# Performance work log

Measured on AMD Instinct MI355X. Metric: run time of the kernel, lower is better.

Reference implementation:

```python
import jax, jax.numpy as jnp
import numpy as np
jax.config.update("jax_enable_x64", True)

B, N, S, H, D = 64, 13, 128, 768, 512
MAX_DEPTH = 8
MAX_SHAPE_IDS = 256  # min(2**13, 256)


def _gelu(x):
    return jax.nn.gelu(x, approximate=False)  # torch nn.GELU default (erf)


def setup_inputs() -> dict:
    key = jax.random.key(0)
    ks = jax.random.split(key, 12)
    # BFS-complete binary tree with 13 nodes: nodes 0..5 internal, 6..12 leaves
    left = np.array([2 * i + 1 if 2 * i + 2 < N else -1 for i in range(N)], dtype=np.int64)
    right = np.array([2 * i + 2 if 2 * i + 2 < N else -1 for i in range(N)], dtype=np.int64)
    depth = np.array([int(np.floor(np.log2(i + 1))) for i in range(N)], dtype=np.int64)
    is_leaf = np.tile((left == -1)[None, :], (B, 1))  # (B, N) bool
    active = np.ones((B, N), dtype=bool)
    leaf_states = jax.random.normal(ks[0], (B, N, S, H), dtype=jnp.float32)
    leaf_masks = jax.random.bernoulli(ks[1], 0.8, (B, N, S))  # bool
    s = 0.02
    params = dict(
        Wl1=jax.random.normal(ks[2], (H, D), dtype=jnp.float32) * s,
        bl1=jnp.zeros((D,), jnp.float32),
        Wl2=jax.random.normal(ks[3], (D, D), dtype=jnp.float32) * s,
        bl2=jnp.zeros((D,), jnp.float32),
        Wm1=jax.random.normal(ks[4], (2 * D, D), dtype=jnp.float32) * s,
        bm1=jnp.zeros((D,), jnp.float32),
        Wm2=jax.random.normal(ks[5], (D, D), dtype=jnp.float32) * s,
        bm2=jnp.zeros((D,), jnp.float32),
        depth_emb=jax.random.normal(ks[6], (MAX_DEPTH, D), dtype=jnp.float32) * s,
        shape_emb=jax.random.normal(ks[7], (MAX_SHAPE_IDS, D), dtype=jnp.float32) * s,
    )
    return dict(is_leaf=is_leaf, active=active, depth=depth, left_child=left,
                right_child=right, leaf_states=leaf_states, leaf_masks=leaf_masks,
                **params)


def reference(is_leaf, active, depth, left_child, right_child, leaf_states, leaf_masks,
              Wl1, bl1, Wl2, bl2, Wm1, bm1, Wm2, bm2, depth_emb, shape_emb):
    is_leaf = jnp.asarray(is_leaf)
    active = jnp.asarray(active)
    # --- leaf pass (vectorized over all nodes) ---
    maskf = leaf_masks[..., None].astype(leaf_states.dtype)          # (B,N,S,1)
    pooled = (leaf_states * maskf).sum(2) / jnp.maximum(maskf.sum(2), 1.0)  # (B,N,H)
    enc = _gelu(pooled @ Wl1 + bl1) @ Wl2 + bl2                       # (B,N,D)
    enc = enc + depth_emb[jnp.asarray(depth)][None, :, :]             # per-node depth embed
    node_repr = enc * is_leaf[..., None].astype(enc.dtype)            # zero non-leaves
    # --- bottom-up merge (small fixed loop over max_nodes, reverse BFS) ---
    lc_np = np.asarray(left_child)
    rc_np = np.asarray(right_child)
    dp_np = np.asarray(depth)
    for i in range(N - 1, -1, -1):
        lc, rc = int(lc_np[i]), int(rc_np[i])
        if lc == -1:
            continue
        is_internal = active[:, i] & ~is_leaf[:, i]                   # (B,)
        cat = jnp.concatenate([node_repr[:, lc], node_repr[:, rc]], axis=-1)  # (B,2D)
        merged = _gelu(cat @ Wm1 + bm1) @ Wm2 + bm2 + depth_emb[int(dp_np[i])]
        # torch code overwrites the whole column with merged*mask iff any internal
        col = jnp.where(jnp.any(is_internal),
                        merged * is_internal[:, None].astype(merged.dtype),
                        node_repr[:, i])
        node_repr = node_repr.at[:, i].set(col)
    # --- topology hash -> shape embedding ---
    pattern = active.astype(jnp.int64) * 2 + is_leaf.astype(jnp.int64)  # (B,N)
    weights = jnp.array([31 ** i for i in range(N)], dtype=jnp.int64)    # fits int64 for N<=13
    hashed = jnp.abs((pattern * weights[None, :]).sum(1)) % MAX_SHAPE_IDS
    return node_repr[:, 0] + shape_emb[hashed]
```

## Files before the change

### kernel.cpp

```cpp
#include <hip/hip_runtime.h>
#include <hip/hip_bf16.h>
#include <math.h>

#define NN 13
#define SS 128
#define HH 768
#define DD 512

typedef __attribute__((ext_vector_type(8))) short bf16x8;
typedef __attribute__((ext_vector_type(4))) float f32x4;

__device__ __forceinline__ float gelu_f(float x) {
    return 0.5f * x * (1.0f + erff(x * 0.7071067811865475f));
}
__device__ __forceinline__ ushort f2b(float v) {
    __hip_bfloat16 h = __float2bfloat16(v);
    return *reinterpret_cast<ushort*>(&h);
}
__device__ __forceinline__ float b2f(ushort u) {
    __hip_bfloat16 h = *reinterpret_cast<__hip_bfloat16*>(&u);
    return __bfloat162float(h);
}

__device__ __forceinline__ int shape_hash(const int* __restrict__ active,
                                          const int* __restrict__ is_leaf, int b) {
    unsigned long long acc = 0ull, w = 1ull;
    for (int i = 0; i < NN; ++i) {
        unsigned long long p = (unsigned long long)(active[b*NN + i] * 2 + is_leaf[b*NN + i]);
        acc += p * w;
        w *= 31ull;
    }
    long long h = (long long)acc;
    if (h < 0) h = -h;
    return (int)(h % 256);
}

__global__ __launch_bounds__(192)
void pool_partial(const float* __restrict__ ls, const int* __restrict__ masks,
                  const int* __restrict__ is_leaf,
                  float* __restrict__ part, float* __restrict__ cntbuf)
{
    int idx = blockIdx.x;
    int R = idx >> 2, q = idx & 3;
    int n = R >> 6, b = R & 63;
    if (!is_leaf[b*NN + n]) return;
    const float4* src = (const float4*)(ls + (size_t)(b*NN + n) * SS * HH + (size_t)q * 32 * HH);
    const int* mk = masks + (b*NN + n) * SS + q * 32;
    int t = threadIdx.x;

    __shared__ float lsm[32];
    if (t < 32) lsm[t] = (float)mk[t];
    __syncthreads();

    float4 a = {0.f, 0.f, 0.f, 0.f};
    float cnt = 0.f;
    #pragma unroll 16
    for (int s = 0; s < 32; ++s) {
        float m = lsm[s];
        float4 v = src[s * (HH/4) + t];
        a.x += m * v.x; a.y += m * v.y; a.z += m * v.z; a.w += m * v.w;
        cnt += m;
    }
    ((float4*)(part + ((size_t)q * 832 + R) * HH))[t] = a;
    if (t == 0) cntbuf[q * 832 + R] = cnt;
}

__global__ __launch_bounds__(256)
void combine_transpose(const float* __restrict__ part, const float* __restrict__ cntbuf,
                       const int* __restrict__ is_leaf, ushort* __restrict__ pooled,
                       const float* __restrict__ Wl1, const float* __restrict__ Wl2,
                       const float* __restrict__ Wm1, const float* __restrict__ Wm2,
                       ushort* __restrict__ Tl1, ushort* __restrict__ Tl2,
                       ushort* __restrict__ Tm1, ushort* __restrict__ Tm2)
{
    int bx = blockIdx.x;
    if (bx < 832) {
        int u = bx;
        int n = u >> 6, b = u & 63;
        int t = threadIdx.x;
        if (t >= 192) return;
        ushort4* dst = (ushort4*)(pooled + (size_t)u * HH);
        if (!is_leaf[b*NN + n]) {
            ushort4 z = {0, 0, 0, 0};
            dst[t] = z;
            return;
        }
        float cnt = cntbuf[u] + cntbuf[832+u] + cntbuf[1664+u] + cntbuf[2496+u];
        float inv = 1.f / fmaxf(cnt, 1.f);
        float4 s = {0.f, 0.f, 0.f, 0.f};
        #pragma unroll
        for (int q = 0; q < 4; ++q) {
            float4 v = ((const float4*)(part + ((size_t)q * 832 + u) * HH))[t];
            s.x += v.x; s.y += v.y; s.z += v.z; s.w += v.w;
        }
        ushort4 o = { f2b(s.x*inv), f2b(s.y*inv), f2b(s.z*inv), f2b(s.w*inv) };
        dst[t] = o;
        return;
    }
    int tb = bx - 832;
    const float* W; ushort* T; int K, tile;
    if (tb < 384)       { W = Wl1; T = Tl1; K = 768;  tile = tb; }
    else if (tb < 640)  { W = Wl2; T = Tl2; K = 512;  tile = tb - 384; }
    else if (tb < 1152) { W = Wm1; T = Tm1; K = 1024; tile = tb - 640; }
    else                { W = Wm2; T = Tm2; K = 512;  tile = tb - 1152; }
    int tk = tile >> 4, tj = tile & 15;
    __shared__ float lds[32][33];
    int t = threadIdx.x;
    int r = t >> 3, c0 = (t & 7) * 4;
    const float4 v = *(const float4*)(W + (size_t)(tk*32 + r)*DD + tj*32 + c0);
    lds[r][c0+0] = v.x; lds[r][c0+1] = v.y; lds[r][c0+2] = v.z; lds[r][c0+3] = v.w;
    __syncthreads();
    ushort* dst = T + (size_t)(tj*32 + r)*K + tk*32 + c0;
    dst[0] = f2b(lds[c0+0][r]); dst[1] = f2b(lds[c0+1][r]);
    dst[2] = f2b(lds[c0+2][r]); dst[3] = f2b(lds[c0+3][r]);
}

enum { LEAF_G1 = 0, LEAF_G2 = 1, MERGE_G1 = 2, MERGE_G2 = 3, FINAL_G2 = 4 };

template<int MODE, int KT>
__global__ __launch_bounds__(256)
void mfma_gemm(const ushort* __restrict__ Asrc, const ushort* __restrict__ WT,
               const float* __restrict__ bias, void* __restrict__ CoutV,
               const int* __restrict__ is_leaf, const int* __restrict__ active,
               const int* __restrict__ depth, const int* __restrict__ left,
               const int* __restrict__ right,
               const float* __restrict__ depth_emb, const float* __restrict__ shape_emb,
               const ushort* __restrict__ noderep,
               int n0, int n1, int n2)
{
    constexpr int NITER = KT / 32;
    __shared__ ushort a_lds[2][64*40];
    __shared__ ushort b_lds[2][64*40];

    const int t = threadIdx.x;
    const int lane = t & 63, wv = t >> 6;
    const int j0 = blockIdx.x * 64;
    const int by = blockIdx.y;
    const int lrow = lane & 15, lhi = lane >> 4;

    int node, lc = 0, rc = 0;
    if (MODE == LEAF_G1 || MODE == LEAF_G2) {
        node = by;
        bool anyleaf = __any(is_leaf[lane*NN + node] != 0);
        if (!anyleaf) {
            if (MODE == LEAF_G2) {
                ushort* dst = (ushort*)CoutV + (size_t)(node*64)*DD;
                #pragma unroll
                for (int c = 0; c < 4; ++c) {
                    int jc = j0 + c*16 + lrow;
                    #pragma unroll
                    for (int reg = 0; reg < 4; ++reg) {
                        int rw = wv*16 + lhi*4 + reg;
                        dst[(size_t)rw*DD + jc] = 0;
                    }
                }
            }
            return;
        }
    } else {
        node = (by == 0) ? n0 : ((by == 1) ? n1 : n2);
        lc = left[node]; rc = right[node];
    }

    const int AK = (MODE == LEAF_G1) ? HH : DD;
    const int rowbase = (MODE == LEAF_G1 || MODE == LEAF_G2) ? node*64
                       : (MODE == MERGE_G1) ? 0 : by*64;

    const int sr = t >> 2, skg = t & 3;
    f32x4 acc[4];
    #pragma unroll
    for (int c = 0; c < 4; ++c) acc[c] = (f32x4){0.f, 0.f, 0.f, 0.f};

    auto addrA = [&](int kt) -> const ushort* {
        int k0 = kt*32 + skg*8;
        if (MODE == MERGE_G1) {
            return (k0 < DD) ? noderep + (size_t)(lc*64 + sr)*DD + k0
                             : noderep + (size_t)(rc*64 + sr)*DD + (k0 - DD);
        }
        return Asrc + (size_t)(rowbase + sr)*AK + k0;
    };
    auto addrB = [&](int kt) -> const ushort* {
        return WT + (size_t)(j0 + sr)*KT + kt*32 + skg*8;
    };

    uint4 aR0, bR0, aR1, bR1;
    auto load0 = [&](int kt) { aR0 = *(const uint4*)addrA(kt); bR0 = *(const uint4*)addrB(kt); };
    auto load1 = [&](int kt) { aR1 = *(const uint4*)addrA(kt); bR1 = *(const uint4*)addrB(kt); };
    auto store0 = [&](int buf) {
        *(uint4*)&a_lds[buf][sr*40 + skg*8] = aR0;
        *(uint4*)&b_lds[buf][sr*40 + skg*8] = bR0;
    };
    auto store1 = [&](int buf) {
        *(uint4*)&a_lds[buf][sr*40 + skg*8] = aR1;
        *(uint4*)&b_lds[buf][sr*40 + skg*8] = bR1;
    };
    auto computeOn = [&](const ushort* aL, const ushort* bL) {
        bf16x8 af = *(const bf16x8*)&aL[(wv*16 + lrow)*40 + lhi*8];
        #pragma unroll
        for (int c = 0; c < 4; ++c) {
            bf16x8 bfr = *(const bf16x8*)&bL[(c*16 + lrow)*40 + lhi*8];
            acc[c] = __builtin_amdgcn_mfma_f32_16x16x32_bf16(af, bfr, acc[c], 0, 0, 0);
        }
    };

    load0(0);
    store0(0);
    if (NITER > 1) load1(1);
    __syncthreads();

    for (int kt = 0; kt < NITER; kt += 2) {
        computeOn(a_lds[0], b_lds[0]);
        if (kt + 2 < NITER) load0(kt + 2);
        store1(1);
        __syncthreads();
        computeOn(a_lds[1], b_lds[1]);
        if (kt + 3 < NITER) load1(kt + 3);
        if (kt + 2 < NITER) store0(0);
        __syncthreads();
    }

    if (MODE == LEAF_G1) {
        ushort* H = (ushort*)CoutV + (size_t)(node*64)*DD;
        #pragma unroll
        for (int c = 0; c < 4; ++c) {
            int jc = j0 + c*16 + lrow;
            float bj = bias[jc];
            #pragma unroll
            for (int reg = 0; reg < 4; ++reg) {
                int rw = wv*16 + lhi*4 + reg;
                H[(size_t)rw*DD + jc] = f2b(gelu_f(acc[c][reg] + bj));
            }
        }
    } else if (MODE == LEAF_G2) {
        int dp = depth[node];
        const float* de = depth_emb + (size_t)dp*DD;
        bool lf[4];
        #pragma unroll
        for (int reg = 0; reg < 4; ++reg)
            lf[reg] = is_leaf[(wv*16 + lhi*4 + reg)*NN + node] != 0;
        ushort* dst = (ushort*)CoutV + (size_t)(node*64)*DD;
        #pragma unroll
        for (int c = 0; c < 4; ++c) {
            int jc = j0 + c*16 + lrow;
            float bj = bias[jc] + de[jc];
            #pragma unroll
            for (int reg = 0; reg < 4; ++reg) {
                int rw = wv*16 + lhi*4 + reg;
                dst[(size_t)rw*DD + jc] = f2b(lf[reg] ? (acc[c][reg] + bj) : 0.f);
            }
        }
    } else if (MODE == MERGE_G1) {
        ushort* Mh = (ushort*)CoutV + (size_t)(by*64)*DD;
        #pragma unroll
        for (int c = 0; c < 4; ++c) {
            int jc = j0 + c*16 + lrow;
            float bj = bias[jc];
            #pragma unroll
            for (int reg = 0; reg < 4; ++reg) {
                int rw = wv*16 + lhi*4 + reg;
                Mh[(size_t)rw*DD + jc] = f2b(gelu_f(acc[c][reg] + bj));
            }
        }
    } else {
        int dp = depth[node];
        const float* de = depth_emb + (size_t)dp*DD;
        bool anyInt = __any(active[lane*NN + node] && !is_leaf[lane*NN + node]);
        bool iv[4];
        #pragma unroll
        for (int reg = 0; reg < 4; ++reg) {
            int rw = wv*16 + lhi*4 + reg;
            iv[reg] = active[rw*NN + node] && !is_leaf[rw*NN + node];
        }
        if (MODE == MERGE_G2) {
            if (!anyInt) return;
            ushort* dst = (ushort*)CoutV + (size_t)(node*64)*DD;
            #pragma unroll
            for (int c = 0; c < 4; ++c) {
                int jc = j0 + c*16 + lrow;
                float bj = bias[jc] + de[jc];
                #pragma unroll
                for (int reg = 0; reg < 4; ++reg) {
                    int rw = wv*16 + lhi*4 + reg;
                    dst[(size_t)rw*DD + jc] = f2b(iv[reg] ? (acc[c][reg] + bj) : 0.f);
                }
            }
        } else {
            float* out = (float*)CoutV;
            int hh[4];
            #pragma unroll
            for (int reg = 0; reg < 4; ++reg)
                hh[reg] = shape_hash(active, is_leaf, wv*16 + lhi*4 + reg);
            #pragma unroll
            for (int c = 0; c < 4; ++c) {
                int jc = j0 + c*16 + lrow;
                float bj = bias[jc] + de[jc];
                #pragma unroll
                for (int reg = 0; reg < 4; ++reg) {
                    int rw = wv*16 + lhi*4 + reg;
                    float base = anyInt ? (iv[reg] ? (acc[c][reg] + bj) : 0.f)
                                        : b2f(noderep[(size_t)(node*64 + rw)*DD + jc]);
                    out[(size_t)rw*DD + jc] = base + shape_emb[(size_t)hh[reg]*DD + jc];
                }
            }
        }
    }
}

extern "C" void kernel_launch(void* const* d_in, const int* in_sizes, int n_in,
                              void* d_out, int out_size, void* d_ws, size_t ws_size,
                              hipStream_t stream)
{
    const int*   is_leaf     = (const int*)d_in[0];
    const int*   active      = (const int*)d_in[1];
    const int*   depth       = (const int*)d_in[2];
    const int*   left        = (const int*)d_in[3];
    const int*   right       = (const int*)d_in[4];
    const float* leaf_states = (const float*)d_in[5];
    const int*   leaf_masks  = (const int*)d_in[6];
    const float* Wl1 = (const float*)d_in[7];
    const float* bl1 = (const float*)d_in[8];
    const float* Wl2 = (const float*)d_in[9];
    const float* bl2 = (const float*)d_in[10];
    const float* Wm1 = (const float*)d_in[11];
    const float* bm1 = (const float*)d_in[12];
    const float* Wm2 = (const float*)d_in[13];
    const float* bm2 = (const float*)d_in[14];
    const float* depth_emb = (const float*)d_in[15];
    const float* shape_emb = (const float*)d_in[16];
    float* out = (float*)d_out;

    float* part   = (float*)d_ws;
    float* cntbuf = part + 4*832*768;
    ushort* pooled  = (ushort*)(cntbuf + 4*832);
    ushort* hidden  = pooled + 832*768;
    ushort* noderep = hidden + 832*512;
    ushort* mhid    = noderep + 832*512;
    ushort* Tl1 = mhid + 3*64*512;
    ushort* Tl2 = Tl1 + 512*768;
    ushort* Tm1 = Tl2 + 512*512;
    ushort* Tm2 = Tm1 + 512*1024;

    pool_partial<<<832*4, 192, 0, stream>>>(leaf_states, leaf_masks, is_leaf, part, cntbuf);
    combine_transpose<<<832 + 1408, 256, 0, stream>>>(part, cntbuf, is_leaf, pooled,
                                                      Wl1, Wl2, Wm1, Wm2, Tl1, Tl2, Tm1, Tm2);

    mfma_gemm<LEAF_G1, 768><<<dim3(8, 13), 256, 0, stream>>>(
        pooled, Tl1, bl1, hidden, is_leaf, active, depth, left, right,
        depth_emb, shape_emb, noderep, 0, 0, 0);
    mfma_gemm<LEAF_G2, 512><<<dim3(8, 13), 256, 0, stream>>>(
        hidden, Tl2, bl2, noderep, is_leaf, active, depth, left, right,
        depth_emb, shape_emb, noderep, 0, 0, 0);

    mfma_gemm<MERGE_G1, 1024><<<dim3(8, 3), 256, 0, stream>>>(
        nullptr, Tm1, bm1, mhid, is_leaf, active, depth, left, right,
        depth_emb, shape_emb, noderep, 3, 4, 5);
    mfma_gemm<MERGE_G2, 512><<<dim3(8, 3), 256, 0, stream>>>(
        mhid, Tm2, bm2, noderep, is_leaf, active, depth, left, right,
        depth_emb, shape_emb, noderep, 3, 4, 5);

    mfma_gemm<MERGE_G1, 1024><<<dim3(8, 2), 256, 0, stream>>>(
        nullptr, Tm1, bm1, mhid, is_leaf, active, depth, left, right,
        depth_emb, shape_emb, noderep, 1, 2, 0);
    mfma_gemm<MERGE_G2, 512><<<dim3(8, 2), 256, 0, stream>>>(
        mhid, Tm2, bm2, noderep, is_leaf, active, depth, left, right,
        depth_emb, shape_emb, noderep, 1, 2, 0);

    mfma_gemm<MERGE_G1, 1024><<<dim3(8, 1), 256, 0, stream>>>(
        nullptr, Tm1, bm1, mhid, is_leaf, active, depth, left, right,
        depth_emb, shape_emb, noderep, 0, 0, 0);
    mfma_gemm<FINAL_G2, 512><<<dim3(8, 1), 256, 0, stream>>>(
        mhid, Tm2, bm2, out, is_leaf, active, depth, left, right,
        depth_emb, shape_emb, noderep, 0, 0, 0);
}
```

Before: 102.7 us.

## Fuse masked pooling into transpose kernel, dropping split-S partial buffer

Removes the separate split-S pooling kernel and its partial-sum workspace. Each leaf row is now pooled by a single block over all 128 sequence positions inside the combined pooling/transpose kernel, which saves a launch and the partial write/read round-trip. In exchange the pooling launch goes from 4x as many blocks (about 3328) to about 448 active leaf blocks, so fewer blocks stream leaf states. Each block also runs a longer serial loop, which may reduce achievable memory bandwidth on the large leaf-state read.

```diff
diff --git a/kernel.cpp b/kernel.cpp
--- a/kernel.cpp
+++ b/kernel.cpp
@@ -35,65 +35,40 @@
     return (int)(h % 256);
 }
 
-__global__ __launch_bounds__(192)
-void pool_partial(const float* __restrict__ ls, const int* __restrict__ masks,
-                  const int* __restrict__ is_leaf,
-                  float* __restrict__ part, float* __restrict__ cntbuf)
-{
-    int idx = blockIdx.x;
-    int R = idx >> 2, q = idx & 3;
-    int n = R >> 6, b = R & 63;
-    if (!is_leaf[b*NN + n]) return;
-    const float4* src = (const float4*)(ls + (size_t)(b*NN + n) * SS * HH + (size_t)q * 32 * HH);
-    const int* mk = masks + (b*NN + n) * SS + q * 32;
-    int t = threadIdx.x;
-
-    __shared__ float lsm[32];
-    if (t < 32) lsm[t] = (float)mk[t];
-    __syncthreads();
-
-    float4 a = {0.f, 0.f, 0.f, 0.f};
-    float cnt = 0.f;
-    #pragma unroll 16
-    for (int s = 0; s < 32; ++s) {
-        float m = lsm[s];
-        float4 v = src[s * (HH/4) + t];
-        a.x += m * v.x; a.y += m * v.y; a.z += m * v.z; a.w += m * v.w;
-        cnt += m;
-    }
-    ((float4*)(part + ((size_t)q * 832 + R) * HH))[t] = a;
-    if (t == 0) cntbuf[q * 832 + R] = cnt;
-}
-
 __global__ __launch_bounds__(256)
-void combine_transpose(const float* __restrict__ part, const float* __restrict__ cntbuf,
-                       const int* __restrict__ is_leaf, ushort* __restrict__ pooled,
-                       const float* __restrict__ Wl1, const float* __restrict__ Wl2,
-                       const float* __restrict__ Wm1, const float* __restrict__ Wm2,
-                       ushort* __restrict__ Tl1, ushort* __restrict__ Tl2,
-                       ushort* __restrict__ Tm1, ushort* __restrict__ Tm2)
+void pool_transpose(const float* __restrict__ ls, const int* __restrict__ masks,
+                    const int* __restrict__ is_leaf, ushort* __restrict__ pooled,
+                    const float* __restrict__ Wl1, const float* __restrict__ Wl2,
+                    const float* __restrict__ Wm1, const float* __restrict__ Wm2,
+                    ushort* __restrict__ Tl1, ushort* __restrict__ Tl2,
+                    ushort* __restrict__ Tm1, ushort* __restrict__ Tm2)
 {
     int bx = blockIdx.x;
+    int t = threadIdx.x;
     if (bx < 832) {
         int u = bx;
         int n = u >> 6, b = u & 63;
-        int t = threadIdx.x;
-        if (t >= 192) return;
         ushort4* dst = (ushort4*)(pooled + (size_t)u * HH);
         if (!is_leaf[b*NN + n]) {
-            ushort4 z = {0, 0, 0, 0};
-            dst[t] = z;
+            if (t < 192) { ushort4 z = {0,0,0,0}; dst[t] = z; }
             return;
         }
-        float cnt = cntbuf[u] + cntbuf[832+u] + cntbuf[1664+u] + cntbuf[2496+u];
+        __shared__ float lsm[SS];
+        if (t < SS) lsm[t] = (float)masks[(b*NN + n)*SS + t];
+        __syncthreads();
+        if (t >= 192) return;
+        const float4* src = (const float4*)(ls + (size_t)(b*NN + n) * SS * HH);
+        float4 a = {0.f, 0.f, 0.f, 0.f};
+        float cnt = 0.f;
+        #pragma unroll 8
+        for (int s = 0; s < SS; ++s) {
+            float m = lsm[s];
+            float4 v = src[s * (HH/4) + t];
+            a.x += m * v.x; a.y += m * v.y; a.z += m * v.z; a.w += m * v.w;
+            cnt += m;
+        }
         float inv = 1.f / fmaxf(cnt, 1.f);
-        float4 s = {0.f, 0.f, 0.f, 0.f};
-        #pragma unroll
-        for (int q = 0; q < 4; ++q) {
-            float4 v = ((const float4*)(part + ((size_t)q * 832 + u) * HH))[t];
-            s.x += v.x; s.y += v.y; s.z += v.z; s.w += v.w;
-        }
-        ushort4 o = { f2b(s.x*inv), f2b(s.y*inv), f2b(s.z*inv), f2b(s.w*inv) };
+        ushort4 o = { f2b(a.x*inv), f2b(a.y*inv), f2b(a.z*inv), f2b(a.w*inv) };
         dst[t] = o;
         return;
     }
@@ -105,7 +80,6 @@
     else                { W = Wm2; T = Tm2; K = 512;  tile = tb - 1152; }
     int tk = tile >> 4, tj = tile & 15;
     __shared__ float lds[32][33];
-    int t = threadIdx.x;
     int r = t >> 3, c0 = (t & 7) * 4;
     const float4 v = *(const float4*)(W + (size_t)(tk*32 + r)*DD + tj*32 + c0);
     lds[r][c0+0] = v.x; lds[r][c0+1] = v.y; lds[r][c0+2] = v.z; lds[r][c0+3] = v.w;
@@ -329,9 +303,7 @@
     const float* shape_emb = (const float*)d_in[16];
     float* out = (float*)d_out;
 
-    float* part   = (float*)d_ws;
-    float* cntbuf = part + 4*832*768;
-    ushort* pooled  = (ushort*)(cntbuf + 4*832);
+    ushort* pooled  = (ushort*)d_ws;
     ushort* hidden  = pooled + 832*768;
     ushort* noderep = hidden + 832*512;
     ushort* mhid    = noderep + 832*512;
@@ -340,9 +312,8 @@
     ushort* Tm1 = Tl2 + 512*512;
     ushort* Tm2 = Tm1 + 512*1024;
 
-    pool_partial<<<832*4, 192, 0, stream>>>(leaf_states, leaf_masks, is_leaf, part, cntbuf);
-    combine_transpose<<<832 + 1408, 256, 0, stream>>>(part, cntbuf, is_leaf, pooled,
-                                                      Wl1, Wl2, Wm1, Wm2, Tl1, Tl2, Tm1, Tm2);
+    pool_transpose<<<832 + 1408, 256, 0, stream>>>(leaf_states, leaf_masks, is_leaf, pooled,
+                                                   Wl1, Wl2, Wm1, Wm2, Tl1, Tl2, Tm1, Tm2);
 
     mfma_gemm<LEAF_G1, 768><<<dim3(8, 13), 256, 0, stream>>>(
         pooled, Tl1, bl1, hidden, is_leaf, active, depth, left, right,
```

After: 99.01 us. 3.6% less time.
